# Optimization experiments

Measured on AMD Instinct MI355X. Metric: run time of the kernel, lower is better.

Reference implementation:

```python
import jax, jax.numpy as jnp
import numpy as np
import math

B, S, E, H, L, VOCAB, OUT = 32, 1024, 512, 8, 2, 20000, 1
D = E // H


def positional_encoding(seq_length, embed_size):
    position = jnp.arange(seq_length, dtype=jnp.float32)[:, None]
    div_term = jnp.exp(jnp.arange(0, embed_size, 2, dtype=jnp.float32) * (-math.log(10000.0) / embed_size))
    pe = jnp.zeros((seq_length, embed_size), dtype=jnp.float32)
    pe = pe.at[:, 0::2].set(jnp.sin(position * div_term))
    pe = pe.at[:, 1::2].set(jnp.cos(position * div_term))
    return pe


def setup_inputs() -> dict:
    key = jax.random.key(0)
    ks = jax.random.split(key, 12)
    inputs = jax.random.randint(ks[0], (B, S), 0, VOCAB)
    s = 1.0 / math.sqrt(E)
    embed_table = jax.random.normal(ks[1], (VOCAB, E), jnp.float32)
    embed_table = embed_table.at[0].set(0.0)  # padding_idx=0
    # per-layer Q,K,V,O linear weights [L,E,E] (applied as x @ W + b) and biases [L,E]
    Wq = jax.random.normal(ks[2], (L, E, E), jnp.float32) * s
    Wk = jax.random.normal(ks[3], (L, E, E), jnp.float32) * s
    Wv = jax.random.normal(ks[4], (L, E, E), jnp.float32) * s
    Wo = jax.random.normal(ks[5], (L, E, E), jnp.float32) * s
    bq = jax.random.normal(ks[6], (L, E), jnp.float32) * s
    bk = jax.random.normal(ks[7], (L, E), jnp.float32) * s
    bv = jax.random.normal(ks[8], (L, E), jnp.float32) * s
    bo = jax.random.normal(ks[9], (L, E), jnp.float32) * s
    W_out = jax.random.normal(ks[10], (E, OUT), jnp.float32) * s
    b_out = jax.random.normal(ks[11], (OUT,), jnp.float32) * s
    return {"inputs": inputs, "embed_table": embed_table, "Wq": Wq, "bq": bq,
            "Wk": Wk, "bk": bk, "Wv": Wv, "bv": bv, "Wo": Wo, "bo": bo,
            "W_out": W_out, "b_out": b_out}


def _mha(x, Wq, bq, Wk, bk, Wv, bv, Wo, bo, mask):
    b, s = x.shape[:2]
    def heads(W, bias):
        return (x @ W + bias).reshape(b, s, H, D).transpose(0, 2, 1, 3)  # [b,H,s,D]
    q, k, v = heads(Wq, bq), heads(Wk, bk), heads(Wv, bv)
    scores = jnp.einsum('bhqd,bhkd->bhqk', q, k) / math.sqrt(D)
    scores = jnp.where(mask, -1e9, scores)
    prob = jax.nn.softmax(scores, axis=-1)
    out = jnp.einsum('bhqk,bhkd->bhqd', prob, v)
    out = out.transpose(0, 2, 1, 3).reshape(b, s, E)
    return out @ Wo + bo


def reference(inputs, embed_table, Wq, bq, Wk, bk, Wv, bv, Wo, bo, W_out, b_out):
    embeds = embed_table[inputs]  # [B,S,E]
    embeds = embeds + positional_encoding(inputs.shape[1], embeds.shape[-1])
    mask = jnp.triu(jnp.ones((inputs.shape[1], inputs.shape[1]), bool), k=1)  # future mask
    out = embeds
    for l in range(L):
        attn = _mha(out, Wq[l], bq[l], Wk[l], bk[l], Wv[l], bv[l], Wo[l], bo[l], mask)
        out = out + jax.nn.relu(attn)  # dropout is identity (eval / p=0)
    return out @ W_out + b_out
```

## Files before the change

### kernel.cpp

```cpp
#include <hip/hip_runtime.h>

typedef unsigned short u16;
typedef unsigned int u32;
using short8  = __attribute__((ext_vector_type(8))) short;
using floatx4 = __attribute__((ext_vector_type(4))) float;

#define NB 32
#define SEQ 1024
#define EMB 512
#define NH 8
#define HD 64
#define NLAYER 2
#define M_ROWS (NB * SEQ)

__device__ __forceinline__ float bf2f(u16 u) {
  union { u32 i; float f; } v; v.i = ((u32)u) << 16; return v.f;
}
__device__ __forceinline__ u16 f2bf(float f) {
  union { float f; u32 i; } v; v.f = f;
  u32 r = v.i + 0x7fffu + ((v.i >> 16) & 1u);
  return (u16)(r >> 16);
}

typedef __attribute__((address_space(3))) unsigned int lds_u32_t;
typedef __attribute__((address_space(1))) const unsigned int gbl_u32_t;
__device__ __forceinline__ void gload16(void* lds, const void* g) {
  gbl_u32_t* gp = (gbl_u32_t*)(unsigned long long)g;
  lds_u32_t* lp = (lds_u32_t*)(unsigned int)(unsigned long long)lds;
  __builtin_amdgcn_global_load_lds(gp, lp, 16, 0, 0);
}

__global__ void prep_weights(const float* __restrict__ Wq, const float* __restrict__ Wk,
                             const float* __restrict__ Wv, const float* __restrict__ Wo,
                             u16* __restrict__ WtQKV, u16* __restrict__ WtO) {
  int idx = blockIdx.x * 256 + threadIdx.x;
  const int QKV_TOT = NLAYER * 3 * EMB * EMB;
  if (idx < QKV_TOT) {
    int l = idx / (3 * EMB * EMB);
    int rem = idx % (3 * EMB * EMB);
    int n = rem / EMB, kk = rem % EMB;
    int w = n >> 9, e = n & 511;
    const float* src = (w == 0) ? Wq : (w == 1) ? Wk : Wv;
    WtQKV[idx] = f2bf(src[((size_t)l * EMB + kk) * EMB + e]);
  } else {
    int j = idx - QKV_TOT;
    int l = j / (EMB * EMB);
    int rem = j % (EMB * EMB);
    int n = rem / EMB, kk = rem % EMB;
    WtO[j] = f2bf(Wo[((size_t)l * EMB + kk) * EMB + n]);
  }
}

__global__ void embed_pe(const int* __restrict__ inp, const float* __restrict__ table,
                         u16* __restrict__ x) {
  int row = blockIdx.x;
  int tok = inp[row];
  int s = row & (SEQ - 1);
  const float negln = -9.210340371976184f / (float)EMB;
  for (int e = threadIdx.x; e < EMB; e += blockDim.x) {
    float val = table[(size_t)tok * EMB + e];
    int i = e >> 1;
    float dt = __expf((float)(2 * i) * negln);
    float ang = (float)s * dt;
    float pe = (e & 1) ? __cosf(ang) : __sinf(ang);
    x[(size_t)row * EMB + e] = f2bf(val + pe);
  }
}

#define BK 32

__global__ __launch_bounds__(256) void gemm_bt(
    const u16* __restrict__ A, const u16* __restrict__ Bt, int K, int mode,
    const float* bias0, const float* bias1, const float* bias2,
    u16* out0, u16* out1, u16* out2, const u16* resid, int Nstride) {
  __shared__ u16 sA[2][128][BK];
  __shared__ u16 sB[2][128][BK];
  int tid = threadIdx.x;
  int wave = tid >> 6, lane = tid & 63;
  int quad = lane >> 4, l16 = lane & 15;
  int wm = wave >> 1, wn = wave & 1;

  int NT = (mode == 0) ? 12 : 4;
  int blk = blockIdx.x;
  int xcd = blk & 7, slot = blk >> 3;
  int mtl = slot / NT, ntl = slot % NT;
  int bm0 = (xcd * 32 + mtl) * 128;
  int bn0 = ntl * 128;
  bool vswap = (mode == 0) && (bn0 >= 1024);

  floatx4 acc[4][4];
#pragma unroll
  for (int i = 0; i < 4; ++i)
#pragma unroll
    for (int j = 0; j < 4; ++j) acc[i][j] = (floatx4){0.f, 0.f, 0.f, 0.f};

  int rb = wave * 32;
  int lrow = lane >> 2;
  int gcg = ((lane & 3) ^ ((lane >> 3) & 3)) * 8;
  int rsl = (quad ^ ((l16 >> 1) & 3)) * 8;

  const u16* Arow0 = &A[(size_t)(bm0 + rb + lrow) * K + gcg];
  const u16* Arow1 = &A[(size_t)(bm0 + rb + 16 + lrow) * K + gcg];
  const u16* Brow0 = &Bt[(size_t)(bn0 + rb + lrow) * K + gcg];
  const u16* Brow1 = &Bt[(size_t)(bn0 + rb + 16 + lrow) * K + gcg];

  gload16(&sA[0][rb][0],      Arow0);
  gload16(&sA[0][rb + 16][0], Arow1);
  gload16(&sB[0][rb][0],      Brow0);
  gload16(&sB[0][rb + 16][0], Brow1);

  const int niter = K / BK;
  int ibuf = 0;
  for (int it = 0; it < niter; ++it) {
    if (it + 1 < niter) {
      int k1 = (it + 1) * BK;
      int nb = ibuf ^ 1;
      gload16(&sA[nb][rb][0],      Arow0 + k1);
      gload16(&sA[nb][rb + 16][0], Arow1 + k1);
      gload16(&sB[nb][rb][0],      Brow0 + k1);
      gload16(&sB[nb][rb + 16][0], Brow1 + k1);
      asm volatile("s_waitcnt vmcnt(4)" ::: "memory");
    } else {
      asm volatile("s_waitcnt vmcnt(0)" ::: "memory");
    }
    asm volatile("s_barrier" ::: "memory");

    short8 af[4], bfr[4];
#pragma unroll
    for (int mi = 0; mi < 4; ++mi)
      af[mi] = *(const short8*)&sA[ibuf][wm * 64 + mi * 16 + l16][rsl];
#pragma unroll
    for (int ni = 0; ni < 4; ++ni)
      bfr[ni] = *(const short8*)&sB[ibuf][wn * 64 + ni * 16 + l16][rsl];
    if (!vswap) {
#pragma unroll
      for (int mi = 0; mi < 4; ++mi)
#pragma unroll
        for (int ni = 0; ni < 4; ++ni)
          acc[mi][ni] = __builtin_amdgcn_mfma_f32_16x16x32_bf16(af[mi], bfr[ni], acc[mi][ni], 0, 0, 0);
    } else {
#pragma unroll
      for (int mi = 0; mi < 4; ++mi)
#pragma unroll
        for (int ni = 0; ni < 4; ++ni)
          acc[mi][ni] = __builtin_amdgcn_mfma_f32_16x16x32_bf16(bfr[ni], af[mi], acc[mi][ni], 0, 0, 0);
    }
    asm volatile("s_waitcnt lgkmcnt(0)" ::: "memory");
    asm volatile("s_barrier" ::: "memory");
    ibuf ^= 1;
  }

  u16* scr = ((u16*)sA) + wave * (16 * 68);
  int erow = lane >> 5;
  int dcol = lane & 31;

  if (!vswap) {
    int w = bn0 >> 9;
    const float* bp = (mode == 1) ? bias0 : ((w == 0) ? bias0 : bias1);
    float sc = (mode == 0 && w == 0) ? 0.125f : 1.0f;
    float bv[4];
#pragma unroll
    for (int ni = 0; ni < 4; ++ni)
      bv[ni] = bp[(bn0 + wn * 64 + ni * 16 + l16) & 511];

#pragma unroll
    for (int mi = 0; mi < 4; ++mi) {
#pragma unroll
      for (int ni = 0; ni < 4; ++ni)
#pragma unroll
        for (int r = 0; r < 4; ++r) {
          float t = (acc[mi][ni][r] + bv[ni]) * sc;
          if (mode == 1) t = fmaxf(t, 0.f);
          scr[(quad * 4 + r) * 68 + ni * 16 + l16] = f2bf(t);
        }
      asm volatile("s_waitcnt lgkmcnt(0)" ::: "memory");

      int m0 = bm0 + wm * 64 + mi * 16;
      int colg = bn0 + wn * 64 + dcol * 2;
#pragma unroll
      for (int p = 0; p < 8; ++p) {
        int row = p * 2 + erow;
        u32 d2 = *(const u32*)&scr[row * 68 + dcol * 2];
        int m = m0 + row;
        if (mode == 0) {
          int e = colg & 511, h = e >> 6, d = e & 63;
          int b = m >> 10, sid = m & 1023;
          u16* optr = (w == 0) ? out0 : out1;
          *(u32*)&optr[((size_t)(b * NH + h) * SEQ + sid) * HD + d] = d2;
        } else {
          size_t off = (size_t)m * Nstride + colg;
          u32 rs = *(const u32*)&resid[off];
          float lo = bf2f((u16)d2) + bf2f((u16)rs);
          float hi = bf2f((u16)(d2 >> 16)) + bf2f((u16)(rs >> 16));
          *(u32*)&out0[off] = ((u32)f2bf(hi) << 16) | f2bf(lo);
        }
      }
      asm volatile("s_waitcnt lgkmcnt(0)" ::: "memory");
    }
  } else {
    float bvv[4][4];
#pragma unroll
    for (int ni = 0; ni < 4; ++ni)
#pragma unroll
      for (int r = 0; r < 4; ++r)
        bvv[ni][r] = bias2[(bn0 + wn * 64 + ni * 16 + quad * 4 + r) & 511];

    int b = (bm0 + wm * 64) >> 10;
    int sid0 = (bm0 + wm * 64) & 1023;
    int n0 = bn0 + wn * 64;
    int h = (n0 >> 6) & 7;
#pragma unroll
    for (int ni = 0; ni < 4; ++ni) {
#pragma unroll
      for (int mi = 0; mi < 4; ++mi)
#pragma unroll
        for (int r = 0; r < 4; ++r)
          scr[(quad * 4 + r) * 68 + mi * 16 + l16] = f2bf(acc[mi][ni][r] + bvv[ni][r]);
      asm volatile("s_waitcnt lgkmcnt(0)" ::: "memory");

      int d0 = (n0 & 63) + ni * 16;
#pragma unroll
      for (int p = 0; p < 8; ++p) {
        int row = p * 2 + erow;
        u32 d2 = *(const u32*)&scr[row * 68 + dcol * 2];
        *(u32*)&out2[((size_t)(b * NH + h) * HD + d0 + row) * SEQ + sid0 + dcol * 2] = d2;
      }
      asm volatile("s_waitcnt lgkmcnt(0)" ::: "memory");
    }
  }
}

__device__ __forceinline__ void stage_tile64(u16 (*dst)[64], const u16* g, int gstride,
                                             int wave, int lane) {
  int r = lane >> 3;
  int gcg = ((lane & 7) ^ r) * 8;
#pragma unroll
  for (int c = 0; c < 2; ++c) {
    int row0 = (wave * 2 + c) * 8;
    gload16(&dst[row0][0], &g[(size_t)(row0 + r) * gstride + gcg]);
  }
}
#define RD8(T, row, cg) (*(const short8*)&T[row][(((cg) ^ ((row) & 7)) * 8)])

__global__ __launch_bounds__(256) void attn_kernel(
    const u16* __restrict__ q, const u16* __restrict__ k, const u16* __restrict__ vt,
    u16* __restrict__ o) {
  int blk = blockIdx.x;
  int xcd = blk & 7, slot = blk >> 3;
  int bh = xcd * 32 + (slot >> 3);
  int qtp = slot & 7;
  int b = bh >> 3, h = bh & 7;
  int qA0 = qtp * 128, qB0 = qA0 + 64;
  __shared__ u16 sQ[128][64], sK[64][64], sV[64][64];
  __shared__ u16 sP[2][64][68];
  int tid = threadIdx.x, wave = tid >> 6, lane = tid & 63;
  int quad = lane >> 4, l16 = lane & 15;

  stage_tile64((u16(*)[64])&sQ[0][0],  &q[((size_t)bh * SEQ + qA0) * HD], HD, wave, lane);
  stage_tile64((u16(*)[64])&sQ[64][0], &q[((size_t)bh * SEQ + qB0) * HD], HD, wave, lane);

  short8 ones;
#pragma unroll
  for (int j = 0; j < 8; ++j) ones[j] = (short)0x3F80;

  floatx4 accoA[4], accoB[4], accsumA, accsumB;
#pragma unroll
  for (int i = 0; i < 4; ++i) {
    accoA[i] = (floatx4){0.f, 0.f, 0.f, 0.f};
    accoB[i] = (floatx4){0.f, 0.f, 0.f, 0.f};
  }
  accsumA = (floatx4){0.f, 0.f, 0.f, 0.f};
  accsumB = (floatx4){0.f, 0.f, 0.f, 0.f};
  short8 aqA0 = {}, aqA1 = {}, aqB0 = {}, aqB1 = {};

  auto process = [&](short8 aq0, short8 aq1, int qX0, bool diag, int sub,
                     floatx4* acco, floatx4& accsum, int k0) {
    floatx4 accs[4];
#pragma unroll
    for (int i = 0; i < 4; ++i) accs[i] = (floatx4){0.f, 0.f, 0.f, 0.f};
#pragma unroll
    for (int nt = 0; nt < 4; ++nt) {
      int rbk = nt * 16 + l16;
      accs[nt] = __builtin_amdgcn_mfma_f32_16x16x32_bf16(aq0, RD8(sK, rbk, quad), accs[nt], 0, 0, 0);
      accs[nt] = __builtin_amdgcn_mfma_f32_16x16x32_bf16(aq1, RD8(sK, rbk, 4 + quad), accs[nt], 0, 0, 0);
    }
    int qg_base = qX0 + wave * 16 + quad * 4;
#pragma unroll
    for (int nt = 0; nt < 4; ++nt) {
      int kg = k0 + nt * 16 + l16;
#pragma unroll
      for (int r = 0; r < 4; ++r) {
        float p = __expf(fminf(accs[nt][r], 75.f));
        if (diag && kg > qg_base + r) p = 0.f;
        sP[sub][wave * 16 + quad * 4 + r][nt * 16 + l16] =
            (u16)(__float_as_uint(p) >> 16);
      }
    }
    asm volatile("s_waitcnt lgkmcnt(0)" ::: "memory");
#pragma unroll
    for (int cst = 0; cst < 2; ++cst) {
      short8 ap = *(const short8*)&sP[sub][wave * 16 + l16][cst * 32 + quad * 8];
#pragma unroll
      for (int dt = 0; dt < 4; ++dt) {
        int rv = dt * 16 + l16;
        acco[dt] = __builtin_amdgcn_mfma_f32_16x16x32_bf16(ap, RD8(sV, rv, cst * 4 + quad), acco[dt], 0, 0, 0);
      }
      accsum = __builtin_amdgcn_mfma_f32_16x16x32_bf16(ap, ones, accsum, 0, 0, 0);
    }
  };

  int ktmax = 2 * qtp + 1;
  for (int kt = 0; kt <= ktmax; ++kt) {
    int k0 = kt * 64;
    __syncthreads();
    stage_tile64(sK, &k[((size_t)bh * SEQ + k0) * HD], HD, wave, lane);
    stage_tile64(sV, &vt[(size_t)bh * HD * SEQ + k0], SEQ, wave, lane);
    __syncthreads();

    if (kt == 0) {
      int ra = wave * 16 + l16;
      aqA0 = RD8(sQ, ra, quad);
      aqA1 = RD8(sQ, ra, 4 + quad);
      int rb_ = 64 + wave * 16 + l16;
      aqB0 = RD8(sQ, rb_, quad);
      aqB1 = RD8(sQ, rb_, 4 + quad);
    }

    if (kt <= 2 * qtp)
      process(aqA0, aqA1, qA0, kt == 2 * qtp, 0, accoA, accsumA, k0);
    process(aqB0, aqB1, qB0, kt == ktmax, 1, accoB, accsumB, k0);
  }

#pragma unroll
  for (int dt = 0; dt < 4; ++dt)
#pragma unroll
    for (int r = 0; r < 4; ++r) {
      int rowoff = wave * 16 + quad * 4 + r;
      int col = h * HD + dt * 16 + l16;
      o[((size_t)b * SEQ + qA0 + rowoff) * EMB + col] = f2bf(accoA[dt][r] / accsumA[r]);
      o[((size_t)b * SEQ + qB0 + rowoff) * EMB + col] = f2bf(accoB[dt][r] / accsumB[r]);
    }
}

__global__ __launch_bounds__(256) void out_proj(const u16* __restrict__ x,
                                                const float* __restrict__ wout,
                                                const float* __restrict__ bout,
                                                float* __restrict__ out) {
  int wave = threadIdx.x >> 6, lane = threadIdx.x & 63;
  int m = blockIdx.x * 4 + wave;
  union { uint4 vv; u16 s[8]; } xv;
  xv.vv = *(const uint4*)&x[(size_t)m * EMB + lane * 8];
  float4 w0 = *(const float4*)&wout[lane * 8];
  float4 w1 = *(const float4*)&wout[lane * 8 + 4];
  float wv[8] = {w0.x, w0.y, w0.z, w0.w, w1.x, w1.y, w1.z, w1.w};
  float s = 0.f;
#pragma unroll
  for (int j = 0; j < 8; ++j) s += bf2f(xv.s[j]) * wv[j];
#pragma unroll
  for (int sh = 1; sh < 64; sh <<= 1) s += __shfl_xor(s, sh, 64);
  if (lane == 0) out[m] = s + bout[0];
}

extern "C" void kernel_launch(void* const* d_in, const int* in_sizes, int n_in,
                              void* d_out, int out_size, void* d_ws, size_t ws_size,
                              hipStream_t stream) {
  const int*   inp   = (const int*)d_in[0];
  const float* table = (const float*)d_in[1];
  const float* Wq    = (const float*)d_in[2];
  const float* bq    = (const float*)d_in[3];
  const float* Wk    = (const float*)d_in[4];
  const float* bk    = (const float*)d_in[5];
  const float* Wv    = (const float*)d_in[6];
  const float* bv    = (const float*)d_in[7];
  const float* Wo    = (const float*)d_in[8];
  const float* bo    = (const float*)d_in[9];
  const float* Wout  = (const float*)d_in[10];
  const float* bout  = (const float*)d_in[11];
  float* outp = (float*)d_out;

  char* ws = (char*)d_ws;
  const size_t SZ = (size_t)M_ROWS * EMB * 2;
  u16* x      = (u16*)(ws);
  u16* qb     = (u16*)(ws + SZ);
  u16* kb     = (u16*)(ws + 2 * SZ);
  u16* vb     = (u16*)(ws + 3 * SZ);
  u16* attn_b = (u16*)(ws + 4 * SZ);
  u16* WtQKV  = (u16*)(ws + 5 * SZ);
  u16* WtO    = (u16*)(ws + 5 * SZ + (size_t)NLAYER * 3 * EMB * EMB * 2);

  prep_weights<<<8192, 256, 0, stream>>>(Wq, Wk, Wv, Wo, WtQKV, WtO);
  embed_pe<<<M_ROWS, 256, 0, stream>>>(inp, table, x);

  for (int l = 0; l < NLAYER; ++l) {
    gemm_bt<<<3072, 256, 0, stream>>>(
        x, WtQKV + (size_t)l * 3 * EMB * EMB, EMB, 0,
        bq + l * EMB, bk + l * EMB, bv + l * EMB, qb, kb, vb, nullptr, 0);
    attn_kernel<<<2048, 256, 0, stream>>>(qb, kb, vb, attn_b);
    gemm_bt<<<1024, 256, 0, stream>>>(
        attn_b, WtO + (size_t)l * EMB * EMB, EMB, 1,
        bo + l * EMB, nullptr, nullptr, x, nullptr, nullptr, x, EMB);
  }
  out_proj<<<8192, 256, 0, stream>>>(x, Wout, bout, outp);
}
```

Measured before the change: 646.3 us.

## Double-buffer K/V tiles in attention, use exp2 with folded log2e scaling

The attention kernel now double-buffers the K and V LDS tiles, prefetching the next tile with async global-to-LDS loads while the current one is processed. This replaces the two-__syncthreads-per-iteration load-then-compute pattern. The Q projection scale now folds in log2(e) so the softmax can use a hardware exp2, and the causal mask check is skipped on non-diagonal tiles. Block order is also reversed so the longest query tiles are scheduled first. The cost is extra LDS for the second buffer, with Q sharing space with K.

```diff
diff --git a/kernel.cpp b/kernel.cpp
--- a/kernel.cpp
+++ b/kernel.cpp
@@ -21,6 +21,12 @@
   u32 r = v.i + 0x7fffu + ((v.i >> 16) & 1u);
   return (u16)(r >> 16);
 }
+
+#if __has_builtin(__builtin_amdgcn_exp2f)
+#define EXP2F __builtin_amdgcn_exp2f
+#else
+#define EXP2F exp2f
+#endif
 
 typedef __attribute__((address_space(3))) unsigned int lds_u32_t;
 typedef __attribute__((address_space(1))) const unsigned int gbl_u32_t;
@@ -157,7 +163,7 @@
   if (!vswap) {
     int w = bn0 >> 9;
     const float* bp = (mode == 1) ? bias0 : ((w == 0) ? bias0 : bias1);
-    float sc = (mode == 0 && w == 0) ? 0.125f : 1.0f;
+    float sc = (mode == 0 && w == 0) ? 0.18033688011112042f : 1.0f;
     float bv[4];
 #pragma unroll
     for (int ni = 0; ni < 4; ++ni)
@@ -230,17 +236,7 @@
   }
 }
 
-__device__ __forceinline__ void stage_tile64(u16 (*dst)[64], const u16* g, int gstride,
-                                             int wave, int lane) {
-  int r = lane >> 3;
-  int gcg = ((lane & 7) ^ r) * 8;
-#pragma unroll
-  for (int c = 0; c < 2; ++c) {
-    int row0 = (wave * 2 + c) * 8;
-    gload16(&dst[row0][0], &g[(size_t)(row0 + r) * gstride + gcg]);
-  }
-}
-#define RD8(T, row, cg) (*(const short8*)&T[row][(((cg) ^ ((row) & 7)) * 8)])
+#define RD8(T, row, cg) (*(const short8*)&(T)[(size_t)(row) * 64 + ((((cg) ^ ((row) & 7))) * 8)])
 
 __global__ __launch_bounds__(256) void attn_kernel(
     const u16* __restrict__ q, const u16* __restrict__ k, const u16* __restrict__ vt,
@@ -248,16 +244,47 @@
   int blk = blockIdx.x;
   int xcd = blk & 7, slot = blk >> 3;
   int bh = xcd * 32 + (slot >> 3);
-  int qtp = slot & 7;
+  int qtp = 7 - (slot & 7);
   int b = bh >> 3, h = bh & 7;
   int qA0 = qtp * 128, qB0 = qA0 + 64;
-  __shared__ u16 sQ[128][64], sK[64][64], sV[64][64];
-  __shared__ u16 sP[2][64][68];
+
+  __shared__ u16 smem[25088];
+  u16* sQ = smem;
+  u16* sK = smem;
+  u16* sV = smem + 8192;
+  u16* sP = smem + 16384;
+
   int tid = threadIdx.x, wave = tid >> 6, lane = tid & 63;
   int quad = lane >> 4, l16 = lane & 15;
-
-  stage_tile64((u16(*)[64])&sQ[0][0],  &q[((size_t)bh * SEQ + qA0) * HD], HD, wave, lane);
-  stage_tile64((u16(*)[64])&sQ[64][0], &q[((size_t)bh * SEQ + qB0) * HD], HD, wave, lane);
+  int rr = lane >> 3, gc8 = ((lane & 7) ^ rr) * 8;
+
+  const u16* qbase = &q[((size_t)bh * SEQ + qA0) * HD];
+  const u16* kbase = &k[(size_t)bh * SEQ * HD];
+  const u16* vbase = &vt[(size_t)bh * HD * SEQ];
+
+#pragma unroll
+  for (int c = 0; c < 2; ++c) {
+    int row0 = wave * 16 + c * 8;
+    gload16(sQ + row0 * 64,        qbase + (size_t)(row0 + rr) * HD + gc8);
+    gload16(sQ + (64 + row0) * 64, qbase + (size_t)(64 + row0 + rr) * HD + gc8);
+  }
+  asm volatile("s_waitcnt vmcnt(0)" ::: "memory");
+  asm volatile("s_barrier" ::: "memory");
+  short8 aqA0, aqA1, aqB0, aqB1;
+  {
+    int ra = wave * 16 + l16;
+    aqA0 = RD8(sQ, ra, quad);
+    aqA1 = RD8(sQ, ra, 4 + quad);
+    aqB0 = RD8(sQ + 4096, ra, quad);
+    aqB1 = RD8(sQ + 4096, ra, 4 + quad);
+  }
+  asm volatile("s_waitcnt lgkmcnt(0)" ::: "memory");
+  asm volatile("s_barrier" ::: "memory");
+
+  const u16* kp0 = kbase + (size_t)(wave * 16 + rr) * HD + gc8;
+  const u16* kp1 = kp0 + 8 * HD;
+  const u16* vp0 = vbase + (size_t)(wave * 16 + rr) * SEQ + gc8;
+  const u16* vp1 = vp0 + 8 * SEQ;
 
   short8 ones;
 #pragma unroll
@@ -271,64 +298,90 @@
   }
   accsumA = (floatx4){0.f, 0.f, 0.f, 0.f};
   accsumB = (floatx4){0.f, 0.f, 0.f, 0.f};
-  short8 aqA0 = {}, aqA1 = {}, aqB0 = {}, aqB1 = {};
 
   auto process = [&](short8 aq0, short8 aq1, int qX0, bool diag, int sub,
-                     floatx4* acco, floatx4& accsum, int k0) {
+                     floatx4* acco, floatx4& accsum, int k0,
+                     const u16* Kc, const u16* Vc) {
     floatx4 accs[4];
 #pragma unroll
     for (int i = 0; i < 4; ++i) accs[i] = (floatx4){0.f, 0.f, 0.f, 0.f};
 #pragma unroll
     for (int nt = 0; nt < 4; ++nt) {
       int rbk = nt * 16 + l16;
-      accs[nt] = __builtin_amdgcn_mfma_f32_16x16x32_bf16(aq0, RD8(sK, rbk, quad), accs[nt], 0, 0, 0);
-      accs[nt] = __builtin_amdgcn_mfma_f32_16x16x32_bf16(aq1, RD8(sK, rbk, 4 + quad), accs[nt], 0, 0, 0);
-    }
-    int qg_base = qX0 + wave * 16 + quad * 4;
-#pragma unroll
-    for (int nt = 0; nt < 4; ++nt) {
-      int kg = k0 + nt * 16 + l16;
-#pragma unroll
-      for (int r = 0; r < 4; ++r) {
-        float p = __expf(fminf(accs[nt][r], 75.f));
-        if (diag && kg > qg_base + r) p = 0.f;
-        sP[sub][wave * 16 + quad * 4 + r][nt * 16 + l16] =
-            (u16)(__float_as_uint(p) >> 16);
+      accs[nt] = __builtin_amdgcn_mfma_f32_16x16x32_bf16(aq0, RD8(Kc, rbk, quad), accs[nt], 0, 0, 0);
+      accs[nt] = __builtin_amdgcn_mfma_f32_16x16x32_bf16(aq1, RD8(Kc, rbk, 4 + quad), accs[nt], 0, 0, 0);
+    }
+    int prowbase = sub * 4352 + (wave * 16 + quad * 4) * 68;
+    if (!diag) {
+#pragma unroll
+      for (int nt = 0; nt < 4; ++nt)
+#pragma unroll
+        for (int r = 0; r < 4; ++r) {
+          float p = EXP2F(fminf(accs[nt][r], 108.f));
+          sP[prowbase + r * 68 + nt * 16 + l16] = (u16)(__float_as_uint(p) >> 16);
+        }
+    } else {
+      int qg_base = qX0 + wave * 16 + quad * 4;
+#pragma unroll
+      for (int nt = 0; nt < 4; ++nt) {
+        int kg = k0 + nt * 16 + l16;
+#pragma unroll
+        for (int r = 0; r < 4; ++r) {
+          float p = EXP2F(fminf(accs[nt][r], 108.f));
+          if (kg > qg_base + r) p = 0.f;
+          sP[prowbase + r * 68 + nt * 16 + l16] = (u16)(__float_as_uint(p) >> 16);
+        }
       }
     }
     asm volatile("s_waitcnt lgkmcnt(0)" ::: "memory");
 #pragma unroll
     for (int cst = 0; cst < 2; ++cst) {
-      short8 ap = *(const short8*)&sP[sub][wave * 16 + l16][cst * 32 + quad * 8];
+      short8 ap = *(const short8*)&sP[sub * 4352 + (wave * 16 + l16) * 68 + cst * 32 + quad * 8];
 #pragma unroll
       for (int dt = 0; dt < 4; ++dt) {
         int rv = dt * 16 + l16;
-        acco[dt] = __builtin_amdgcn_mfma_f32_16x16x32_bf16(ap, RD8(sV, rv, cst * 4 + quad), acco[dt], 0, 0, 0);
+        acco[dt] = __builtin_amdgcn_mfma_f32_16x16x32_bf16(ap, RD8(Vc, rv, cst * 4 + quad), acco[dt], 0, 0, 0);
       }
       accsum = __builtin_amdgcn_mfma_f32_16x16x32_bf16(ap, ones, accsum, 0, 0, 0);
     }
   };
 
+  {
+    int row0 = wave * 16;
+    gload16(sK + row0 * 64,       kp0);
+    gload16(sK + (row0 + 8) * 64, kp1);
+    gload16(sV + row0 * 64,       vp0);
+    gload16(sV + (row0 + 8) * 64, vp1);
+  }
+
   int ktmax = 2 * qtp + 1;
+  int cur = 0;
   for (int kt = 0; kt <= ktmax; ++kt) {
+    if (kt < ktmax) {
+      int nb = cur ^ 1;
+      size_t ko = (size_t)(kt + 1) * (64 * HD);
+      size_t vo = (size_t)(kt + 1) * 64;
+      int row0 = wave * 16;
+      gload16(sK + nb * 4096 + row0 * 64,       kp0 + ko);
+      gload16(sK + nb * 4096 + (row0 + 8) * 64, kp1 + ko);
+      gload16(sV + nb * 4096 + row0 * 64,       vp0 + vo);
+      gload16(sV + nb * 4096 + (row0 + 8) * 64, vp1 + vo);
+      asm volatile("s_waitcnt vmcnt(4)" ::: "memory");
+    } else {
+      asm volatile("s_waitcnt vmcnt(0)" ::: "memory");
+    }
+    asm volatile("s_barrier" ::: "memory");
+
+    const u16* Kc = sK + cur * 4096;
+    const u16* Vc = sV + cur * 4096;
     int k0 = kt * 64;
-    __syncthreads();
-    stage_tile64(sK, &k[((size_t)bh * SEQ + k0) * HD], HD, wave, lane);
-    stage_tile64(sV, &vt[(size_t)bh * HD * SEQ + k0], SEQ, wave, lane);
-    __syncthreads();
-
-    if (kt == 0) {
-      int ra = wave * 16 + l16;
-      aqA0 = RD8(sQ, ra, quad);
-      aqA1 = RD8(sQ, ra, 4 + quad);
-      int rb_ = 64 + wave * 16 + l16;
-      aqB0 = RD8(sQ, rb_, quad);
-      aqB1 = RD8(sQ, rb_, 4 + quad);
-    }
-
     if (kt <= 2 * qtp)
-      process(aqA0, aqA1, qA0, kt == 2 * qtp, 0, accoA, accsumA, k0);
-    process(aqB0, aqB1, qB0, kt == ktmax, 1, accoB, accsumB, k0);
+      process(aqA0, aqA1, qA0, kt == 2 * qtp, 0, accoA, accsumA, k0, Kc, Vc);
+    process(aqB0, aqB1, qB0, kt == ktmax, 1, accoB, accsumB, k0, Kc, Vc);
+
+    asm volatile("s_waitcnt lgkmcnt(0)" ::: "memory");
+    asm volatile("s_barrier" ::: "memory");
+    cur ^= 1;
   }
 
 #pragma unroll
```

Result: slower. 688.7 us (+6.5%).
